# Kernel optimization log

Hardware: AMD Instinct MI355X
Metric: run time of the kernel (lower is better)

Reference implementation:

```python
import jax, jax.numpy as jnp
import numpy as np

EPS = 1e-5


def _conv(x, w, padding=0, dilation=1, groups=1):
    return jax.lax.conv_general_dilated(
        x, w, window_strides=(1, 1),
        padding=[(padding, padding), (padding, padding)],
        rhs_dilation=(dilation, dilation),
        dimension_numbers=('NCHW', 'OIHW', 'NCHW'),
        feature_group_count=groups)


def _bn(x, gamma, beta, mean, var):
    # eval-mode BatchNorm2d over channel dim (NCHW)
    scale = (gamma * jax.lax.rsqrt(var + EPS))[None, :, None, None]
    shift = (beta - mean * gamma * jax.lax.rsqrt(var + EPS))[None, :, None, None]
    return x * scale + shift


def setup_inputs() -> dict:
    key = jax.random.key(0)
    B, Cin, H, W = 16, 256, 64, 64
    Chid, Cout = 256, 256
    ks = [3, 5, 7, 9]
    keys = jax.random.split(key, 32)
    ki = iter(keys)

    def rn(shape, scale=0.05):
        return jax.random.normal(next(ki), shape, dtype=jnp.float32) * scale

    inp = {'x': jax.random.normal(next(ki), (B, Cin, H, W), dtype=jnp.float32)}
    # pre_conv: 1x1 conv (no bias) + BN + ReLU
    inp['pre_w'] = rn((Chid, Cin, 1, 1))
    inp['bn1_g'] = 1.0 + rn((Chid,))
    inp['bn1_b'] = rn((Chid,))
    inp['bn1_m'] = rn((Chid,))
    inp['bn1_v'] = jnp.abs(1.0 + rn((Chid,)))
    # depthwise convs k=3,5,7,9 (bias, no BN)
    for k in ks:
        inp[f'dw{k}_w'] = rn((Chid, 1, k, k))
        inp[f'dw{k}_b'] = rn((Chid,))
    # pw_conv: 1x1 + BN + ReLU
    inp['pw_w'] = rn((Chid, Chid, 1, 1))
    inp['bn2_g'] = 1.0 + rn((Chid,))
    inp['bn2_b'] = rn((Chid,))
    inp['bn2_m'] = rn((Chid,))
    inp['bn2_v'] = jnp.abs(1.0 + rn((Chid,)))
    # post_conv: 1x1 + BN + ReLU
    inp['post_w'] = rn((Cout, Chid, 1, 1))
    inp['bn3_g'] = 1.0 + rn((Cout,))
    inp['bn3_b'] = rn((Cout,))
    inp['bn3_m'] = rn((Cout,))
    inp['bn3_v'] = jnp.abs(1.0 + rn((Cout,)))
    return inp


def reference(x, pre_w, bn1_g, bn1_b, bn1_m, bn1_v,
              dw3_w, dw3_b, dw5_w, dw5_b, dw7_w, dw7_b, dw9_w, dw9_b,
              pw_w, bn2_g, bn2_b, bn2_m, bn2_v,
              post_w, bn3_g, bn3_b, bn3_m, bn3_v):
    C = pre_w.shape[0]
    # pre_conv
    h = jax.nn.relu(_bn(_conv(x, pre_w), bn1_g, bn1_b, bn1_m, bn1_v))
    # sum of identity + 4 depthwise branches (same-padded)
    s = h
    for k, w, b in ((3, dw3_w, dw3_b), (5, dw5_w, dw5_b),
                    (7, dw7_w, dw7_b), (9, dw9_w, dw9_b)):
        s = s + _conv(h, w, padding=(k - 1) // 2, groups=C) + b[None, :, None, None]
    # pw_conv then post_conv
    s = jax.nn.relu(_bn(_conv(s, pw_w), bn2_g, bn2_b, bn2_m, bn2_v))
    out = jax.nn.relu(_bn(_conv(s, post_w), bn3_g, bn3_b, bn3_m, bn3_v))
    return out
```

## Files before the change

kernel.cpp:

```cpp
#include <hip/hip_runtime.h>
#include <stdint.h>

#define HW 4096
#define CCH 256
#define BPL (CCH * HW)
#define LSTR 264
#define TILE 64
#define NT 4
#define DSTR 84

typedef __attribute__((ext_vector_type(8))) short short8;
typedef __attribute__((ext_vector_type(4))) float floatx4;
typedef unsigned short ushort_t;

__device__ inline ushort_t f2bf(float f) {
    union { float f; unsigned int u; } v; v.f = f;
    unsigned int r = v.u + 0x7FFFu + ((v.u >> 16) & 1u);
    return (ushort_t)(r >> 16);
}
__device__ inline void up2(unsigned int d, float* w) {
    union { unsigned int u; float f; } lo, hi;
    lo.u = d << 16; hi.u = d & 0xffff0000u;
    w[0] = lo.f; w[1] = hi.f;
}

__device__ inline int wpack(int c, int t) {
    const int w  = c >> 6, mt = (c >> 4) & 3, L = c & 15;
    const int kt = t >> 5, quad = (t >> 3) & 3, e = t & 7;
    return ((((w * 8 + kt) * 4 + mt) * 64 + quad * 16 + L) * 8 + e);
}

__global__ void prep_kernel(
    const float* __restrict__ pre_w, const float* __restrict__ pw_w, const float* __restrict__ post_w,
    const float* __restrict__ g1, const float* __restrict__ b1, const float* __restrict__ m1, const float* __restrict__ v1,
    const float* __restrict__ g2, const float* __restrict__ b2, const float* __restrict__ m2, const float* __restrict__ v2,
    const float* __restrict__ g3, const float* __restrict__ b3, const float* __restrict__ m3, const float* __restrict__ v3,
    const float* __restrict__ w3d, const float* __restrict__ b3d,
    const float* __restrict__ w5d, const float* __restrict__ b5d,
    const float* __restrict__ w7d, const float* __restrict__ b7d,
    const float* __restrict__ w9d, const float* __restrict__ b9d,
    ushort_t* __restrict__ w1b, ushort_t* __restrict__ w2b, ushort_t* __restrict__ w3b,
    float* __restrict__ WcP, float* __restrict__ biasc,
    float* __restrict__ sc1, float* __restrict__ sh1,
    float* __restrict__ sc2, float* __restrict__ sh2,
    float* __restrict__ sc3, float* __restrict__ sh3)
{
    int c = blockIdx.x, t = threadIdx.x;
    const int p = wpack(c, t);
    w1b[p] = f2bf(pre_w[c * 256 + t]);
    w2b[p] = f2bf(pw_w[c * 256 + t]);
    w3b[p] = f2bf(post_w[c * 256 + t]);
    if (t < 128) {
        float val = 0.f;
        int dy = -1, dx = 0;
        if (t < 45) { dy = t / 9; dx = t % 9; }
        else if (t >= 64 && t < 100) { int i = t - 64; dy = 5 + i / 9; dx = i % 9; }
        if (dy >= 0) {
            val = w9d[c * 81 + dy * 9 + dx];
            if (dy >= 1 && dy <= 7 && dx >= 1 && dx <= 7) val += w7d[c * 49 + (dy - 1) * 7 + (dx - 1)];
            if (dy >= 2 && dy <= 6 && dx >= 2 && dx <= 6) val += w5d[c * 25 + (dy - 2) * 5 + (dx - 2)];
            if (dy >= 3 && dy <= 5 && dx >= 3 && dx <= 5) val += w3d[c * 9 + (dy - 3) * 3 + (dx - 3)];
            if (dy == 4 && dx == 4) val += 1.0f;
        }
        WcP[c * 128 + t] = val;
    }
    if (t == 128) { float s = g1[c] * rsqrtf(v1[c] + 1e-5f); sc1[c] = s; sh1[c] = b1[c] - m1[c] * s; }
    if (t == 129) { float s = g2[c] * rsqrtf(v2[c] + 1e-5f); sc2[c] = s; sh2[c] = b2[c] - m2[c] * s; }
    if (t == 130) { float s = g3[c] * rsqrtf(v3[c] + 1e-5f); sc3[c] = s; sh3[c] = b3[c] - m3[c] * s; }
    if (t == 131) biasc[c] = b3d[c] + b5d[c] + b7d[c] + b9d[c];
}

template <int MODE>
__global__ __launch_bounds__(256, 4) void conv_tile(
    const void* __restrict__ inp,
    const ushort_t* __restrict__ wA, const float* __restrict__ scA, const float* __restrict__ shA,
    const ushort_t* __restrict__ wB, const float* __restrict__ scB, const float* __restrict__ shB,
    void* __restrict__ outp)
{
    __shared__ __align__(16) ushort_t Bs[TILE * LSTR];
    const int tid = threadIdx.x;
    const int P0 = blockIdx.x * TILE;
    const int b = P0 >> 12, hw0 = P0 & 4095;
    unsigned int* Bsd = (unsigned int*)Bs;

    {
        const int c2 = tid & 127, ph = tid >> 7, px0 = ph * 32;
        if (MODE == 0) {
            const float* s0 = (const float*)inp + (size_t)b * BPL + (size_t)(2 * c2) * HW + hw0 + px0;
            const float* s1 = s0 + HW;
#pragma unroll
            for (int i = 0; i < 8; i++) {
                float4 v0 = *(const float4*)(s0 + 4 * i);
                float4 v1 = *(const float4*)(s1 + 4 * i);
                const int px = px0 + 4 * i;
                Bsd[(px + 0) * (LSTR / 2) + c2] = (unsigned)f2bf(v0.x) | ((unsigned)f2bf(v1.x) << 16);
                Bsd[(px + 1) * (LSTR / 2) + c2] = (unsigned)f2bf(v0.y) | ((unsigned)f2bf(v1.y) << 16);
                Bsd[(px + 2) * (LSTR / 2) + c2] = (unsigned)f2bf(v0.z) | ((unsigned)f2bf(v1.z) << 16);
                Bsd[(px + 3) * (LSTR / 2) + c2] = (unsigned)f2bf(v0.w) | ((unsigned)f2bf(v1.w) << 16);
            }
        } else {
            const ushort_t* s0 = (const ushort_t*)inp + (size_t)b * BPL + (size_t)(2 * c2) * HW + hw0 + px0;
            const ushort_t* s1 = s0 + HW;
#pragma unroll
            for (int i = 0; i < 4; i++) {
                union { uint4 v; ushort_t u[8]; } r0, r1;
                r0.v = *(const uint4*)(s0 + 8 * i);
                r1.v = *(const uint4*)(s1 + 8 * i);
                const int px = px0 + 8 * i;
#pragma unroll
                for (int j = 0; j < 8; j++)
                    Bsd[(px + j) * (LSTR / 2) + c2] = (unsigned)r0.u[j] | ((unsigned)r1.u[j] << 16);
            }
        }
    }
    __syncthreads();

    const int wave = tid >> 6, lane = tid & 63, quad = lane >> 4, L = lane & 15;
    const int coutw = wave * 64;

    floatx4 acc[4][NT];

    auto run_gemm = [&](const ushort_t* W) {
#pragma unroll
        for (int mt = 0; mt < 4; mt++)
#pragma unroll
            for (int nt = 0; nt < NT; nt++) acc[mt][nt] = (floatx4){0.f, 0.f, 0.f, 0.f};
        const ushort_t* Ab = W + (size_t)wave * 16384 + (size_t)lane * 8;
        short8 Ac[4], An[4];
#pragma unroll
        for (int mt = 0; mt < 4; mt++) Ac[mt] = *(const short8*)(Ab + mt * 512);
#pragma unroll
        for (int kt = 0; kt < 8; kt++) {
            if (kt < 7) {
#pragma unroll
                for (int mt = 0; mt < 4; mt++)
                    An[mt] = *(const short8*)(Ab + ((kt + 1) * 4 + mt) * 512);
            }
            short8 Bf[NT];
#pragma unroll
            for (int nt = 0; nt < NT; nt++)
                Bf[nt] = *(const short8*)&Bs[(nt * 16 + L) * LSTR + kt * 32 + quad * 8];
            __builtin_amdgcn_s_setprio(1);
#pragma unroll
            for (int mt = 0; mt < 4; mt++)
#pragma unroll
                for (int nt = 0; nt < NT; nt++)
                    acc[mt][nt] = __builtin_amdgcn_mfma_f32_16x16x32_bf16(
                        Ac[mt], Bf[nt], acc[mt][nt], 0, 0, 0);
            __builtin_amdgcn_s_setprio(0);
            if (kt < 7) {
#pragma unroll
                for (int mt = 0; mt < 4; mt++) Ac[mt] = An[mt];
            }
        }
    };

    run_gemm(wA);

    if (MODE == 0) {
        ushort_t* outb = (ushort_t*)outp + (size_t)b * BPL + hw0;
#pragma unroll
        for (int mt = 0; mt < 4; mt++) {
#pragma unroll
            for (int r = 0; r < 4; r++) {
                const int cout = coutw + mt * 16 + quad * 4 + r;
                const float s = scA[cout], h0 = shA[cout];
#pragma unroll
                for (int nt = 0; nt < NT; nt++)
                    outb[(size_t)cout * HW + nt * 16 + L] =
                        f2bf(fmaxf(fmaf(acc[mt][nt][r], s, h0), 0.f));
            }
        }
    } else {
        __syncthreads();
#pragma unroll
        for (int mt = 0; mt < 4; mt++) {
            const int cout0 = coutw + mt * 16 + quad * 4;
            float sc4[4], sh4[4];
#pragma unroll
            for (int r = 0; r < 4; r++) { sc4[r] = scA[cout0 + r]; sh4[r] = shA[cout0 + r]; }
#pragma unroll
            for (int nt = 0; nt < NT; nt++) {
                const int px = nt * 16 + L;
                ushort4 pk;
                pk.x = f2bf(fmaxf(fmaf(acc[mt][nt][0], sc4[0], sh4[0]), 0.f));
                pk.y = f2bf(fmaxf(fmaf(acc[mt][nt][1], sc4[1], sh4[1]), 0.f));
                pk.z = f2bf(fmaxf(fmaf(acc[mt][nt][2], sc4[2], sh4[2]), 0.f));
                pk.w = f2bf(fmaxf(fmaf(acc[mt][nt][3], sc4[3], sh4[3]), 0.f));
                *(ushort4*)&Bs[px * LSTR + cout0] = pk;
            }
        }
        __syncthreads();
        run_gemm(wB);
        float* outb = (float*)outp + (size_t)b * BPL + hw0;
#pragma unroll
        for (int mt = 0; mt < 4; mt++) {
#pragma unroll
            for (int r = 0; r < 4; r++) {
                const int cout = coutw + mt * 16 + quad * 4 + r;
                const float s = scB[cout], h0 = shB[cout];
#pragma unroll
                for (int nt = 0; nt < NT; nt++)
                    outb[(size_t)cout * HW + nt * 16 + L] =
                        fmaxf(fmaf(acc[mt][nt][r], s, h0), 0.f);
            }
        }
    }
}

__global__ __launch_bounds__(256, 3) void dw_kernel(
    const ushort_t* __restrict__ h, const float* __restrict__ WcP,
    const float* __restrict__ biasc, ushort_t* __restrict__ out)
{
    const int bcp = blockIdx.x, c = bcp & 255;
    const size_t plane = (size_t)bcp * HW;
    __shared__ __align__(16) ushort_t tile[72 * DSTR];
    const int tid = threadIdx.x;

    for (int f = tid; f < 272; f += 256) {
        int row, col;
        if (f < 144) { int rr = f / 18; row = (rr < 4) ? rr : rr + 64; col = 4 + (f % 18) * 4; }
        else { int f2 = f - 144; row = 4 + (f2 >> 1); col = (f2 & 1) ? 72 : 4; }
        *(uint2*)&tile[row * DSTR + col] = make_uint2(0u, 0u);
    }
    {
        const int r = tid >> 2, q = tid & 3;
        const ushort_t* src = h + plane + r * 64 + q * 16;
        uint4 a = *(const uint4*)src;
        uint4 b = *(const uint4*)(src + 8);
        ushort_t* drow = &tile[(r + 4) * DSTR + 8 + q * 16];
        *(uint2*)(drow + 0)  = make_uint2(a.x, a.y);
        *(uint2*)(drow + 4)  = make_uint2(a.z, a.w);
        *(uint2*)(drow + 8)  = make_uint2(b.x, b.y);
        *(uint2*)(drow + 12) = make_uint2(b.z, b.w);
    }
    __syncthreads();

    const int tx = tid & 15, ty = tid >> 4;
    const int x0 = tx * 4, y0 = ty * 4;
    float acc[4][4];
#pragma unroll
    for (int i = 0; i < 4; i++)
#pragma unroll
        for (int j = 0; j < 4; j++) acc[i][j] = 0.f;

    const float* wp = WcP + c * 128;
    float wr[48];

    auto ldrow = [&](int r6, float* win) {
        const ushort_t* rp = &tile[(y0 + r6) * DSTR + x0 + 4];
        uint2 a = *(const uint2*)rp;
        uint2 b = *(const uint2*)(rp + 4);
        uint2 c2 = *(const uint2*)(rp + 8);
        up2(a.x, win + 0);  up2(a.y, win + 2);
        up2(b.x, win + 4);  up2(b.y, win + 6);
        up2(c2.x, win + 8); up2(c2.y, win + 10);
    };

#pragma unroll
    for (int i = 0; i < 12; i++) *(float4*)&wr[4 * i] = *(const float4*)(wp + 4 * i);
#pragma unroll
    for (int r6 = 0; r6 < 8; r6++) {
        float win[12];
        ldrow(r6, win);
#pragma unroll
        for (int yy = 0; yy < 4; yy++) {
            const int d = r6 - yy;
            if (d >= 0 && d <= 4) {
#pragma unroll
                for (int t = 0; t < 9; t++)
#pragma unroll
                    for (int j = 0; j < 4; j++)
                        acc[yy][j] = fmaf(wr[d * 9 + t], win[j + t], acc[yy][j]);
            }
        }
    }
#pragma unroll
    for (int i = 0; i < 9; i++) *(float4*)&wr[4 * i] = *(const float4*)(wp + 64 + 4 * i);
#pragma unroll
    for (int r6 = 5; r6 < 12; r6++) {
        float win[12];
        ldrow(r6, win);
#pragma unroll
        for (int yy = 0; yy < 4; yy++) {
            const int d = r6 - yy;
            if (d >= 5 && d <= 8) {
#pragma unroll
                for (int t = 0; t < 9; t++)
#pragma unroll
                    for (int j = 0; j < 4; j++)
                        acc[yy][j] = fmaf(wr[(d - 5) * 9 + t], win[j + t], acc[yy][j]);
            }
        }
    }

    const float bb = biasc[c];
#pragma unroll
    for (int yy = 0; yy < 4; yy++) {
        ushort4 o;
        o.x = f2bf(acc[yy][0] + bb);
        o.y = f2bf(acc[yy][1] + bb);
        o.z = f2bf(acc[yy][2] + bb);
        o.w = f2bf(acc[yy][3] + bb);
        *(ushort4*)&out[plane + (size_t)(y0 + yy) * 64 + x0] = o;
    }
}

extern "C" void kernel_launch(void* const* d_in, const int* in_sizes, int n_in,
                              void* d_out, int out_size, void* d_ws, size_t ws_size,
                              hipStream_t stream) {
    const float* x     = (const float*)d_in[0];
    const float* pre_w = (const float*)d_in[1];
    const float* bn1g  = (const float*)d_in[2];
    const float* bn1b  = (const float*)d_in[3];
    const float* bn1m  = (const float*)d_in[4];
    const float* bn1v  = (const float*)d_in[5];
    const float* dw3w  = (const float*)d_in[6];
    const float* dw3b  = (const float*)d_in[7];
    const float* dw5w  = (const float*)d_in[8];
    const float* dw5b  = (const float*)d_in[9];
    const float* dw7w  = (const float*)d_in[10];
    const float* dw7b  = (const float*)d_in[11];
    const float* dw9w  = (const float*)d_in[12];
    const float* dw9b  = (const float*)d_in[13];
    const float* pww   = (const float*)d_in[14];
    const float* bn2g  = (const float*)d_in[15];
    const float* bn2b  = (const float*)d_in[16];
    const float* bn2m  = (const float*)d_in[17];
    const float* bn2v  = (const float*)d_in[18];
    const float* postw = (const float*)d_in[19];
    const float* bn3g  = (const float*)d_in[20];
    const float* bn3b  = (const float*)d_in[21];
    const float* bn3m  = (const float*)d_in[22];
    const float* bn3v  = (const float*)d_in[23];

    char* wsb = (char*)d_ws;
    ushort_t* sbuf = (ushort_t*)wsb;
    ushort_t* hbuf = (ushort_t*)d_out;
    char* aux = wsb + (size_t)33 * 1024 * 1024;
    ushort_t* w1b = (ushort_t*)aux;
    ushort_t* w2b = w1b + 65536;
    ushort_t* w3b = w2b + 65536;
    float* WcP   = (float*)(w3b + 65536);
    float* biasc = WcP + 256 * 128;
    float* sc1 = biasc + 256;  float* sh1 = sc1 + 256;
    float* sc2 = sh1 + 256;    float* sh2 = sc2 + 256;
    float* sc3 = sh2 + 256;    float* sh3 = sc3 + 256;

    prep_kernel<<<256, 256, 0, stream>>>(
        pre_w, pww, postw,
        bn1g, bn1b, bn1m, bn1v, bn2g, bn2b, bn2m, bn2v, bn3g, bn3b, bn3m, bn3v,
        dw3w, dw3b, dw5w, dw5b, dw7w, dw7b, dw9w, dw9b,
        w1b, w2b, w3b, WcP, biasc, sc1, sh1, sc2, sh2, sc3, sh3);

    const int nconv = (16 * HW) / TILE;
    conv_tile<0><<<nconv, 256, 0, stream>>>(x, w1b, sc1, sh1,
                                            nullptr, nullptr, nullptr, hbuf);
    dw_kernel<<<16 * CCH, 256, 0, stream>>>(hbuf, WcP, biasc, sbuf);
    conv_tile<1><<<nconv, 256, 0, stream>>>(sbuf, w2b, sc2, sh2,
                                            w3b, sc3, sh3, (float*)d_out);
}
```

Measured before the change: 231.0 us.

## Process two tiles per block and prefetch the second into registers

```diff
diff --git a/kernel.cpp b/kernel.cpp
--- a/kernel.cpp
+++ b/kernel.cpp
@@ -71,7 +71,7 @@
 }
 
 template <int MODE>
-__global__ __launch_bounds__(256, 4) void conv_tile(
+__global__ __launch_bounds__(256, 2) void conv_tile(
     const void* __restrict__ inp,
     const ushort_t* __restrict__ wA, const float* __restrict__ scA, const float* __restrict__ shA,
     const ushort_t* __restrict__ wB, const float* __restrict__ scB, const float* __restrict__ shB,
@@ -79,17 +79,112 @@
 {
     __shared__ __align__(16) ushort_t Bs[TILE * LSTR];
     const int tid = threadIdx.x;
-    const int P0 = blockIdx.x * TILE;
-    const int b = P0 >> 12, hw0 = P0 & 4095;
     unsigned int* Bsd = (unsigned int*)Bs;
+    const int c2 = tid & 127, ph = tid >> 7, px0 = ph * (TILE / 2);
+    const int wave = tid >> 6, lane = tid & 63, quad = lane >> 4, L = lane & 15;
+    const int coutw = wave * 64;
+
+    floatx4 acc[4][NT];
+
+    auto run_gemm = [&](const ushort_t* W) {
+#pragma unroll
+        for (int mt = 0; mt < 4; mt++)
+#pragma unroll
+            for (int nt = 0; nt < NT; nt++) acc[mt][nt] = (floatx4){0.f, 0.f, 0.f, 0.f};
+        const ushort_t* Ab = W + (size_t)wave * 16384 + (size_t)lane * 8;
+        short8 Ac[4], An[4];
+#pragma unroll
+        for (int mt = 0; mt < 4; mt++) Ac[mt] = *(const short8*)(Ab + mt * 512);
+#pragma unroll
+        for (int kt = 0; kt < 8; kt++) {
+            if (kt < 7) {
+#pragma unroll
+                for (int mt = 0; mt < 4; mt++)
+                    An[mt] = *(const short8*)(Ab + ((kt + 1) * 4 + mt) * 512);
+            }
+            short8 Bf[NT];
+#pragma unroll
+            for (int nt = 0; nt < NT; nt++)
+                Bf[nt] = *(const short8*)&Bs[(nt * 16 + L) * LSTR + kt * 32 + quad * 8];
+            __builtin_amdgcn_s_setprio(1);
+#pragma unroll
+            for (int mt = 0; mt < 4; mt++)
+#pragma unroll
+                for (int nt = 0; nt < NT; nt++)
+                    acc[mt][nt] = __builtin_amdgcn_mfma_f32_16x16x32_bf16(
+                        Ac[mt], Bf[nt], acc[mt][nt], 0, 0, 0);
+            __builtin_amdgcn_s_setprio(0);
+            if (kt < 7) {
+#pragma unroll
+                for (int mt = 0; mt < 4; mt++) Ac[mt] = An[mt];
+            }
+        }
+    };
+
+    auto process = [&](int P0) {
+        const int b = P0 >> 12, hw0 = P0 & 4095;
+        run_gemm(wA);
+        if (MODE == 0) {
+            ushort_t* outb = (ushort_t*)outp + (size_t)b * BPL + hw0;
+#pragma unroll
+            for (int mt = 0; mt < 4; mt++) {
+#pragma unroll
+                for (int r = 0; r < 4; r++) {
+                    const int cout = coutw + mt * 16 + quad * 4 + r;
+                    const float s = scA[cout], h0 = shA[cout];
+#pragma unroll
+                    for (int nt = 0; nt < NT; nt++)
+                        outb[(size_t)cout * HW + nt * 16 + L] =
+                            f2bf(fmaxf(fmaf(acc[mt][nt][r], s, h0), 0.f));
+                }
+            }
+        } else {
+            __syncthreads();
+#pragma unroll
+            for (int mt = 0; mt < 4; mt++) {
+                const int cout0 = coutw + mt * 16 + quad * 4;
+                float sc4[4], sh4[4];
+#pragma unroll
+                for (int r = 0; r < 4; r++) { sc4[r] = scA[cout0 + r]; sh4[r] = shA[cout0 + r]; }
+#pragma unroll
+                for (int nt = 0; nt < NT; nt++) {
+                    const int px = nt * 16 + L;
+                    ushort4 pk;
+                    pk.x = f2bf(fmaxf(fmaf(acc[mt][nt][0], sc4[0], sh4[0]), 0.f));
+                    pk.y = f2bf(fmaxf(fmaf(acc[mt][nt][1], sc4[1], sh4[1]), 0.f));
+                    pk.z = f2bf(fmaxf(fmaf(acc[mt][nt][2], sc4[2], sh4[2]), 0.f));
+                    pk.w = f2bf(fmaxf(fmaf(acc[mt][nt][3], sc4[3], sh4[3]), 0.f));
+                    *(ushort4*)&Bs[px * LSTR + cout0] = pk;
+                }
+            }
+            __syncthreads();
+            run_gemm(wB);
+            float* outb = (float*)outp + (size_t)b * BPL + hw0;
+#pragma unroll
+            for (int mt = 0; mt < 4; mt++) {
+#pragma unroll
+                for (int r = 0; r < 4; r++) {
+                    const int cout = coutw + mt * 16 + quad * 4 + r;
+                    const float s = scB[cout], h0 = shB[cout];
+#pragma unroll
+                    for (int nt = 0; nt < NT; nt++)
+                        outb[(size_t)cout * HW + nt * 16 + L] =
+                            fmaxf(fmaf(acc[mt][nt][r], s, h0), 0.f);
+                }
+            }
+        }
+    };
+
+    const int P0 = blockIdx.x * (2 * TILE);
+    const int P1 = P0 + TILE;
 
     {
-        const int c2 = tid & 127, ph = tid >> 7, px0 = ph * 32;
+        const int b = P0 >> 12, hw0 = P0 & 4095;
         if (MODE == 0) {
             const float* s0 = (const float*)inp + (size_t)b * BPL + (size_t)(2 * c2) * HW + hw0 + px0;
             const float* s1 = s0 + HW;
 #pragma unroll
-            for (int i = 0; i < 8; i++) {
+            for (int i = 0; i < TILE / 8; i++) {
                 float4 v0 = *(const float4*)(s0 + 4 * i);
                 float4 v1 = *(const float4*)(s1 + 4 * i);
                 const int px = px0 + 4 * i;
@@ -102,7 +197,7 @@
             const ushort_t* s0 = (const ushort_t*)inp + (size_t)b * BPL + (size_t)(2 * c2) * HW + hw0 + px0;
             const ushort_t* s1 = s0 + HW;
 #pragma unroll
-            for (int i = 0; i < 4; i++) {
+            for (int i = 0; i < TILE / 16; i++) {
                 union { uint4 v; ushort_t u[8]; } r0, r1;
                 r0.v = *(const uint4*)(s0 + 8 * i);
                 r1.v = *(const uint4*)(s1 + 8 * i);
@@ -115,120 +210,81 @@
     }
     __syncthreads();
 
-    const int wave = tid >> 6, lane = tid & 63, quad = lane >> 4, L = lane & 15;
-    const int coutw = wave * 64;
-
-    floatx4 acc[4][NT];
-
-    auto run_gemm = [&](const ushort_t* W) {
-#pragma unroll
-        for (int mt = 0; mt < 4; mt++)
-#pragma unroll
-            for (int nt = 0; nt < NT; nt++) acc[mt][nt] = (floatx4){0.f, 0.f, 0.f, 0.f};
-        const ushort_t* Ab = W + (size_t)wave * 16384 + (size_t)lane * 8;
-        short8 Ac[4], An[4];
-#pragma unroll
-        for (int mt = 0; mt < 4; mt++) Ac[mt] = *(const short8*)(Ab + mt * 512);
-#pragma unroll
-        for (int kt = 0; kt < 8; kt++) {
-            if (kt < 7) {
-#pragma unroll
-                for (int mt = 0; mt < 4; mt++)
-                    An[mt] = *(const short8*)(Ab + ((kt + 1) * 4 + mt) * 512);
-            }
-            short8 Bf[NT];
-#pragma unroll
-            for (int nt = 0; nt < NT; nt++)
-                Bf[nt] = *(const short8*)&Bs[(nt * 16 + L) * LSTR + kt * 32 + quad * 8];
-            __builtin_amdgcn_s_setprio(1);
-#pragma unroll
-            for (int mt = 0; mt < 4; mt++)
-#pragma unroll
-                for (int nt = 0; nt < NT; nt++)
-                    acc[mt][nt] = __builtin_amdgcn_mfma_f32_16x16x32_bf16(
-                        Ac[mt], Bf[nt], acc[mt][nt], 0, 0, 0);
-            __builtin_amdgcn_s_setprio(0);
-            if (kt < 7) {
-#pragma unroll
-                for (int mt = 0; mt < 4; mt++) Ac[mt] = An[mt];
-            }
-        }
-    };
-
-    run_gemm(wA);
+    float4 pa[8], pb[8];
+    uint4  qa[4], qb[4];
+    {
+        const int b = P1 >> 12, hw0 = P1 & 4095;
+        if (MODE == 0) {
+            const float* s0 = (const float*)inp + (size_t)b * BPL + (size_t)(2 * c2) * HW + hw0 + px0;
+            const float* s1 = s0 + HW;
+#pragma unroll
+            for (int i = 0; i < 8; i++) {
+                pa[i] = *(const float4*)(s0 + 4 * i);
+                pb[i] = *(const float4*)(s1 + 4 * i);
+            }
+        } else {
+            const ushort_t* s0 = (const ushort_t*)inp + (size_t)b * BPL + (size_t)(2 * c2) * HW + hw0 + px0;
+            const ushort_t* s1 = s0 + HW;
+#pragma unroll
+            for (int i = 0; i < 4; i++) {
+                qa[i] = *(const uint4*)(s0 + 8 * i);
+                qb[i] = *(const uint4*)(s1 + 8 * i);
+            }
+        }
+    }
+
+    process(P0);
+
+    __syncthreads();
 
     if (MODE == 0) {
-        ushort_t* outb = (ushort_t*)outp + (size_t)b * BPL + hw0;
-#pragma unroll
-        for (int mt = 0; mt < 4; mt++) {
-#pragma unroll
-            for (int r = 0; r < 4; r++) {
-                const int cout = coutw + mt * 16 + quad * 4 + r;
-                const float s = scA[cout], h0 = shA[cout];
-#pragma unroll
-                for (int nt = 0; nt < NT; nt++)
-                    outb[(size_t)cout * HW + nt * 16 + L] =
-                        f2bf(fmaxf(fmaf(acc[mt][nt][r], s, h0), 0.f));
-            }
+#pragma unroll
+        for (int i = 0; i < 8; i++) {
+            const int px = px0 + 4 * i;
+            Bsd[(px + 0) * (LSTR / 2) + c2] = (unsigned)f2bf(pa[i].x) | ((unsigned)f2bf(pb[i].x) << 16);
+            Bsd[(px + 1) * (LSTR / 2) + c2] = (unsigned)f2bf(pa[i].y) | ((unsigned)f2bf(pb[i].y) << 16);
+            Bsd[(px + 2) * (LSTR / 2) + c2] = (unsigned)f2bf(pa[i].z) | ((unsigned)f2bf(pb[i].z) << 16);
+            Bsd[(px + 3) * (LSTR / 2) + c2] = (unsigned)f2bf(pa[i].w) | ((unsigned)f2bf(pb[i].w) << 16);
         }
     } else {
-        __syncthreads();
-#pragma unroll
-        for (int mt = 0; mt < 4; mt++) {
-            const int cout0 = coutw + mt * 16 + quad * 4;
-            float sc4[4], sh4[4];
-#pragma unroll
-            for (int r = 0; r < 4; r++) { sc4[r] = scA[cout0 + r]; sh4[r] = shA[cout0 + r]; }
-#pragma unroll
-            for (int nt = 0; nt < NT; nt++) {
-                const int px = nt * 16 + L;
-                ushort4 pk;
-                pk.x = f2bf(fmaxf(fmaf(acc[mt][nt][0], sc4[0], sh4[0]), 0.f));
-                pk.y = f2bf(fmaxf(fmaf(acc[mt][nt][1], sc4[1], sh4[1]), 0.f));
-                pk.z = f2bf(fmaxf(fmaf(acc[mt][nt][2], sc4[2], sh4[2]), 0.f));
-                pk.w = f2bf(fmaxf(fmaf(acc[mt][nt][3], sc4[3], sh4[3]), 0.f));
-                *(ushort4*)&Bs[px * LSTR + cout0] = pk;
-            }
-        }
-        __syncthreads();
-        run_gemm(wB);
-        float* outb = (float*)outp + (size_t)b * BPL + hw0;
-#pragma unroll
-        for (int mt = 0; mt < 4; mt++) {
-#pragma unroll
-            for (int r = 0; r < 4; r++) {
-                const int cout = coutw + mt * 16 + quad * 4 + r;
-                const float s = scB[cout], h0 = shB[cout];
-#pragma unroll
-                for (int nt = 0; nt < NT; nt++)
-                    outb[(size_t)cout * HW + nt * 16 + L] =
-                        fmaxf(fmaf(acc[mt][nt][r], s, h0), 0.f);
-            }
-        }
-    }
-}
-
-__global__ __launch_bounds__(256, 3) void dw_kernel(
+#pragma unroll
+        for (int i = 0; i < 4; i++) {
+            union { uint4 v; ushort_t u[8]; } r0, r1;
+            r0.v = qa[i]; r1.v = qb[i];
+            const int px = px0 + 8 * i;
+#pragma unroll
+            for (int j = 0; j < 8; j++)
+                Bsd[(px + j) * (LSTR / 2) + c2] = (unsigned)r0.u[j] | ((unsigned)r1.u[j] << 16);
+        }
+    }
+    __syncthreads();
+
+    process(P1);
+}
+
+__global__ __launch_bounds__(256, 4) void dw_kernel(
     const ushort_t* __restrict__ h, const float* __restrict__ WcP,
     const float* __restrict__ biasc, ushort_t* __restrict__ out)
 {
-    const int bcp = blockIdx.x, c = bcp & 255;
-    const size_t plane = (size_t)bcp * HW;
-    __shared__ __align__(16) ushort_t tile[72 * DSTR];
+    const int bcp0 = blockIdx.x * 2;
+    __shared__ __align__(16) ushort_t tA[72 * DSTR], tB[72 * DSTR];
     const int tid = threadIdx.x;
 
-    for (int f = tid; f < 272; f += 256) {
+    for (int f = tid; f < 544; f += 256) {
+        const int g = (f >= 272) ? f - 272 : f;
+        ushort_t* T = (f >= 272) ? tB : tA;
         int row, col;
-        if (f < 144) { int rr = f / 18; row = (rr < 4) ? rr : rr + 64; col = 4 + (f % 18) * 4; }
-        else { int f2 = f - 144; row = 4 + (f2 >> 1); col = (f2 & 1) ? 72 : 4; }
-        *(uint2*)&tile[row * DSTR + col] = make_uint2(0u, 0u);
-    }
+        if (g < 144) { int rr = g / 18; row = (rr < 4) ? rr : rr + 64; col = 4 + (g % 18) * 4; }
+        else { int g2 = g - 144; row = 4 + (g2 >> 1); col = (g2 & 1) ? 72 : 4; }
+        *(uint2*)&T[row * DSTR + col] = make_uint2(0u, 0u);
+    }
+
+    const int r = tid >> 2, q = tid & 3;
     {
-        const int r = tid >> 2, q = tid & 3;
-        const ushort_t* src = h + plane + r * 64 + q * 16;
+        const ushort_t* src = h + (size_t)bcp0 * HW + r * 64 + q * 16;
         uint4 a = *(const uint4*)src;
         uint4 b = *(const uint4*)(src + 8);
-        ushort_t* drow = &tile[(r + 4) * DSTR + 8 + q * 16];
+        ushort_t* drow = &tA[(r + 4) * DSTR + 8 + q * 16];
         *(uint2*)(drow + 0)  = make_uint2(a.x, a.y);
         *(uint2*)(drow + 4)  = make_uint2(a.z, a.w);
         *(uint2*)(drow + 8)  = make_uint2(b.x, b.y);
@@ -236,74 +292,99 @@
     }
     __syncthreads();
 
+    uint4 p1a, p1b;
+    {
+        const ushort_t* src = h + (size_t)(bcp0 + 1) * HW + r * 64 + q * 16;
+        p1a = *(const uint4*)src;
+        p1b = *(const uint4*)(src + 8);
+    }
+
     const int tx = tid & 15, ty = tid >> 4;
     const int x0 = tx * 4, y0 = ty * 4;
-    float acc[4][4];
-#pragma unroll
-    for (int i = 0; i < 4; i++)
-#pragma unroll
-        for (int j = 0; j < 4; j++) acc[i][j] = 0.f;
-
-    const float* wp = WcP + c * 128;
-    float wr[48];
-
-    auto ldrow = [&](int r6, float* win) {
-        const ushort_t* rp = &tile[(y0 + r6) * DSTR + x0 + 4];
-        uint2 a = *(const uint2*)rp;
-        uint2 b = *(const uint2*)(rp + 4);
-        uint2 c2 = *(const uint2*)(rp + 8);
-        up2(a.x, win + 0);  up2(a.y, win + 2);
-        up2(b.x, win + 4);  up2(b.y, win + 6);
-        up2(c2.x, win + 8); up2(c2.y, win + 10);
+
+    auto compute_store = [&](const ushort_t* tile, int bcp) {
+        const int c = bcp & 255;
+        const size_t plane = (size_t)bcp * HW;
+        float acc[4][4];
+#pragma unroll
+        for (int i = 0; i < 4; i++)
+#pragma unroll
+            for (int j = 0; j < 4; j++) acc[i][j] = 0.f;
+
+        const float* wp = WcP + c * 128;
+        float wr[48];
+
+        auto ldrow = [&](int r6, float* win) {
+            const ushort_t* rp = &tile[(y0 + r6) * DSTR + x0 + 4];
+            uint2 a = *(const uint2*)rp;
+            uint2 b = *(const uint2*)(rp + 4);
+            uint2 c2 = *(const uint2*)(rp + 8);
+            up2(a.x, win + 0);  up2(a.y, win + 2);
+            up2(b.x, win + 4);  up2(b.y, win + 6);
+            up2(c2.x, win + 8); up2(c2.y, win + 10);
+        };
+
+#pragma unroll
+        for (int i = 0; i < 12; i++) *(float4*)&wr[4 * i] = *(const float4*)(wp + 4 * i);
+#pragma unroll
+        for (int r6 = 0; r6 < 8; r6++) {
+            float win[12];
+            ldrow(r6, win);
+#pragma unroll
+            for (int yy = 0; yy < 4; yy++) {
+                const int d = r6 - yy;
+                if (d >= 0 && d <= 4) {
+#pragma unroll
+                    for (int t = 0; t < 9; t++)
+#pragma unroll
+                        for (int j = 0; j < 4; j++)
+                            acc[yy][j] = fmaf(wr[d * 9 + t], win[j + t], acc[yy][j]);
+                }
+            }
+        }
+#pragma unroll
+        for (int i = 0; i < 9; i++) *(float4*)&wr[4 * i] = *(const float4*)(wp + 64 + 4 * i);
+#pragma unroll
+        for (int r6 = 5; r6 < 12; r6++) {
+            float win[12];
+            ldrow(r6, win);
+#pragma unroll
+            for (int yy = 0; yy < 4; yy++) {
+                const int d = r6 - yy;
+                if (d >= 5 && d <= 8) {
+#pragma unroll
+                    for (int t = 0; t < 9; t++)
+#pragma unroll
+                        for (int j = 0; j < 4; j++)
+                            acc[yy][j] = fmaf(wr[(d - 5) * 9 + t], win[j + t], acc[yy][j]);
+                }
+            }
+        }
+
+        const float bb = biasc[c];
+#pragma unroll
+        for (int yy = 0; yy < 4; yy++) {
+            ushort4 o;
+            o.x = f2bf(acc[yy][0] + bb);
+            o.y = f2bf(acc[yy][1] + bb);
+            o.z = f2bf(acc[yy][2] + bb);
+            o.w = f2bf(acc[yy][3] + bb);
+            *(ushort4*)&out[plane + (size_t)(y0 + yy) * 64 + x0] = o;
+        }
     };
 
-#pragma unroll
-    for (int i = 0; i < 12; i++) *(float4*)&wr[4 * i] = *(const float4*)(wp + 4 * i);
-#pragma unroll
-    for (int r6 = 0; r6 < 8; r6++) {
-        float win[12];
-        ldrow(r6, win);
-#pragma unroll
-        for (int yy = 0; yy < 4; yy++) {
-            const int d = r6 - yy;
-            if (d >= 0 && d <= 4) {
-#pragma unroll
-                for (int t = 0; t < 9; t++)
-#pragma unroll
-                    for (int j = 0; j < 4; j++)
-                        acc[yy][j] = fmaf(wr[d * 9 + t], win[j + t], acc[yy][j]);
-            }
-        }
-    }
-#pragma unroll
-    for (int i = 0; i < 9; i++) *(float4*)&wr[4 * i] = *(const float4*)(wp + 64 + 4 * i);
-#pragma unroll
-    for (int r6 = 5; r6 < 12; r6++) {
-        float win[12];
-        ldrow(r6, win);
-#pragma unroll
-        for (int yy = 0; yy < 4; yy++) {
-            const int d = r6 - yy;
-            if (d >= 5 && d <= 8) {
-#pragma unroll
-                for (int t = 0; t < 9; t++)
-#pragma unroll
-                    for (int j = 0; j < 4; j++)
-                        acc[yy][j] = fmaf(wr[(d - 5) * 9 + t], win[j + t], acc[yy][j]);
-            }
-        }
-    }
-
-    const float bb = biasc[c];
-#pragma unroll
-    for (int yy = 0; yy < 4; yy++) {
-        ushort4 o;
-        o.x = f2bf(acc[yy][0] + bb);
-        o.y = f2bf(acc[yy][1] + bb);
-        o.z = f2bf(acc[yy][2] + bb);
-        o.w = f2bf(acc[yy][3] + bb);
-        *(ushort4*)&out[plane + (size_t)(y0 + yy) * 64 + x0] = o;
-    }
+    compute_store(tA, bcp0);
+
+    {
+        ushort_t* drow = &tB[(r + 4) * DSTR + 8 + q * 16];
+        *(uint2*)(drow + 0)  = make_uint2(p1a.x, p1a.y);
+        *(uint2*)(drow + 4)  = make_uint2(p1a.z, p1a.w);
+        *(uint2*)(drow + 8)  = make_uint2(p1b.x, p1b.y);
+        *(uint2*)(drow + 12) = make_uint2(p1b.z, p1b.w);
+    }
+    __syncthreads();
+
+    compute_store(tB, bcp0 + 1);
 }
 
 extern "C" void kernel_launch(void* const* d_in, const int* in_sizes, int n_in,
@@ -353,10 +434,10 @@
         dw3w, dw3b, dw5w, dw5b, dw7w, dw7b, dw9w, dw9b,
         w1b, w2b, w3b, WcP, biasc, sc1, sh1, sc2, sh2, sc3, sh3);
 
-    const int nconv = (16 * HW) / TILE;
+    const int nconv = (16 * HW) / (2 * TILE);
     conv_tile<0><<<nconv, 256, 0, stream>>>(x, w1b, sc1, sh1,
                                             nullptr, nullptr, nullptr, hbuf);
-    dw_kernel<<<16 * CCH, 256, 0, stream>>>(hbuf, WcP, biasc, sbuf);
+    dw_kernel<<<8 * CCH, 256, 0, stream>>>(hbuf, WcP, biasc, sbuf);
     conv_tile<1><<<nconv, 256, 0, stream>>>(sbuf, w2b, sc2, sh2,
                                             w3b, sc3, sh3, (float*)d_out);
 }
```

Result: slower. 297.4 us (+28.8%).
